# Performance work log

Hardware: AMD Instinct MI355X
Metric: run time of the kernel (lower is better)

## Reference

```python
import jax, jax.numpy as jnp
import numpy as np

N = 320   # batch of events
D = 64    # features per event
P = 1000  # permutation_count (hard-coded in module)


def setup_inputs() -> dict:
    key = jax.random.key(0)
    k1, k2, k3 = jax.random.split(key, 3)
    data = jax.random.normal(k1, (N, D), dtype=jnp.float32)
    particle_types = jax.random.randint(k2, (N,), 0, 2, dtype=jnp.int32)
    # quantum permutations: 1000 independent random permutations of [0, N)
    perms = jax.vmap(lambda k: jax.random.permutation(k, N))(jax.random.split(k3, P)).astype(jnp.int32)
    return {
        "data": data,
        "fermion_antisymmetry": jnp.float32(-1.0),
        "boson_symmetry": jnp.float32(1.0),
        "particle_types": particle_types,
        "perms": perms,
    }


def reference(data, fermion_antisymmetry, boson_symmetry, particle_types, perms):
    n = data.shape[0]
    tf = particle_types  # [n]
    # statistics factor matrix F[i,j]: fermion-fermion -> -1 param, boson-boson -> +1 param, mixed -> 1.0
    ff = (tf[:, None] == 0) & (tf[None, :] == 0)
    bb = (tf[:, None] == 1) & (tf[None, :] == 1)
    F = jnp.where(ff, fermion_antisymmetry, jnp.where(bb, boson_symmetry, jnp.float32(1.0)))  # [n,n]

    ar = jnp.arange(n)
    gathered = data[perms]                      # [P,n,d] = data[perm[i]]
    fac = F[ar[None, :], perms]                 # [P,n]   = F[i, perm[i]]
    same = perms == ar[None, :]                 # i == perm[i]: keep original row unscaled
    perm_data = jnp.where(same[..., None], gathered, fac[..., None] * gathered)  # [P,n,d]

    all_data = jnp.concatenate([data[None], perm_data], axis=0)  # [P+1,n,d]; row 0 = original

    # pairwise Euclidean norms via Gram trick (avoids [P+1,n,n,d] diff tensor)
    sn = jnp.sum(all_data * all_data, axis=-1)                   # [P+1,n]
    gram = jnp.einsum('pnd,pmd->pnm', all_data, all_data)        # [P+1,n,n]
    sq = jnp.maximum(sn[:, :, None] + sn[:, None, :] - 2.0 * gram, 0.0)

    iu, ju = jnp.triu_indices(n, k=1)
    vals = F[iu, ju][None, :] * jnp.sqrt(sq[:, iu, ju])          # [P+1, n*(n-1)/2]
    # torch.var default is unbiased (ddof=1)
    stats = jnp.var(vals, axis=1, ddof=1)                        # [P+1]
    return stats  # stats[0] = original test statistic, stats[1:] = permutation null distribution
```

## Files before the change

### kernel.cpp

```cpp
#include <hip/hip_runtime.h>
#include <math.h>

#define NN 320
#define DD 64
#define NPAIRF ((double)(NN * (NN - 1) / 2))

__global__ __launch_bounds__(NN) void gram_kernel(const float* __restrict__ data,
                                                  float* __restrict__ G) {
    __shared__ float rowa[DD];
    const int a = blockIdx.x;
    const int t = threadIdx.x;
    if (t < DD) rowa[t] = data[a * DD + t];
    __syncthreads();
    const float* rb = data + t * DD;
    float s = 0.f;
#pragma unroll
    for (int k = 0; k < DD; k += 4) {
        float4 x = *(const float4*)(rb + k);
        s = fmaf(rowa[k + 0], x.x, s);
        s = fmaf(rowa[k + 1], x.y, s);
        s = fmaf(rowa[k + 2], x.z, s);
        s = fmaf(rowa[k + 3], x.w, s);
    }
    G[a * NN + t] = s;
}

__global__ __launch_bounds__(512, 8) void perm_kernel(const float* __restrict__ G,
                                                      const int* __restrict__ types,
                                                      const int* __restrict__ perms,
                                                      const float* __restrict__ fermp,
                                                      const float* __restrict__ bosp,
                                                      float* __restrict__ out) {
    __shared__ __align__(16) float apk[NN * 4];
    __shared__ __align__(16) float colu[NN];
    __shared__ __align__(16) float colusn[NN];
    __shared__ __align__(16) float colvF[NN];
    __shared__ __align__(16) float colvB[NN];
    __shared__ double rsv[8], rsv2[8];

    const int p = blockIdx.x;
    const int t = threadIdx.x;
    const float Fv = *fermp;
    const float Bv = *bosp;
    const int* prow = (p == 0) ? (const int*)nullptr : perms + (size_t)(p - 1) * NN;

    for (int i = t; i < NN; i += 512) {
        const int a  = prow ? prow[i] : i;
        const int ti = types[i];
        const int ta = types[a];
        float uv = 1.0f;
        if (a != i) uv = (ti == 0 && ta == 0) ? Fv : ((ti == 1 && ta == 1) ? Bv : 1.0f);
        colu[a]  = uv;
        colvF[a] = (ti == 0) ? Fv : 1.0f;
        colvB[a] = (ti == 1) ? Bv : 1.0f;
        apk[4 * a + 0] = uv;
        apk[4 * a + 2] = -2.0f * uv;
        apk[4 * a + 3] = (float)ti;
    }
    __syncthreads();
    for (int a = t; a < NN; a += 512) {
        const float uv  = colu[a];
        const float usn = uv * uv * G[a * NN + a];
        colusn[a] = usn;
        apk[4 * a + 1] = usn;
    }
    __syncthreads();

    float accv = 0.0f, acc2 = 0.0f;

    const int strip  = t % 40;
    const int rowoff = t / 40;

    if (rowoff < 12) {
        const int col0 = strip * 8;
        const float4 ub0   = *(const float4*)(colu   + col0);
        const float4 ub1   = *(const float4*)(colu   + col0 + 4);
        const float4 usnb0 = *(const float4*)(colusn + col0);
        const float4 usnb1 = *(const float4*)(colusn + col0 + 4);
        const float4 vFb0  = *(const float4*)(colvF  + col0);
        const float4 vFb1  = *(const float4*)(colvF  + col0 + 4);
        const float4 vBb0  = *(const float4*)(colvB  + col0);
        const float4 vBb1  = *(const float4*)(colvB  + col0 + 4);

        const float* gp  = G + rowoff * NN + col0;
        const float* app = apk + 4 * rowoff;

#define PAIR_BODY(GC, UBC, USNBC, VFC, VBC)                      \
        {                                                        \
            const float tt  = (UBC) * (GC);                      \
            const float sab = ap.y + (USNBC);                    \
            const float d2  = fmaf(ap.z, tt, sab);               \
            const float dd  = __builtin_amdgcn_sqrtf(fabsf(d2)); \
            const float vsl = wa1 ? (VBC) : (VFC);               \
            accv = fmaf(vsl, dd, accv);                          \
            acc2 += fabsf(d2);                                   \
        }

#define ROW_BODY()                                               \
        {                                                        \
            const float4 ap = *(const float4*)app;               \
            const bool wa1 = (ap.w != 0.0f);                     \
            const float4 g0 = *(const float4*)gp;                \
            const float4 g1 = *(const float4*)(gp + 4);          \
            PAIR_BODY(g0.x, ub0.x, usnb0.x, vFb0.x, vBb0.x)      \
            PAIR_BODY(g0.y, ub0.y, usnb0.y, vFb0.y, vBb0.y)      \
            PAIR_BODY(g0.z, ub0.z, usnb0.z, vFb0.z, vBb0.z)      \
            PAIR_BODY(g0.w, ub0.w, usnb0.w, vFb0.w, vBb0.w)      \
            PAIR_BODY(g1.x, ub1.x, usnb1.x, vFb1.x, vBb1.x)      \
            PAIR_BODY(g1.y, ub1.y, usnb1.y, vFb1.y, vBb1.y)      \
            PAIR_BODY(g1.z, ub1.z, usnb1.z, vFb1.z, vBb1.z)      \
            PAIR_BODY(g1.w, ub1.w, usnb1.w, vFb1.w, vBb1.w)      \
        }

#pragma unroll 2
        for (int it = 0; it < 26; ++it) {
            ROW_BODY();
            gp  += 12 * NN;
            app += 48;
        }
        if (rowoff < 8) {
            ROW_BODY();
        }
#undef ROW_BODY
#undef PAIR_BODY
    }

    double sv = (double)accv, sv2 = (double)acc2;
    for (int off = 32; off; off >>= 1) {
        sv  += __shfl_down(sv, off, 64);
        sv2 += __shfl_down(sv2, off, 64);
    }
    const int wid = t >> 6, lane = t & 63;
    if (lane == 0) { rsv[wid] = sv; rsv2[wid] = sv2; }
    __syncthreads();
    if (t == 0) {
        double SV = 0.0, SV2 = 0.0;
#pragma unroll
        for (int i = 0; i < 8; ++i) { SV += rsv[i]; SV2 += rsv2[i]; }
        SV  *= 0.5;
        SV2 *= 0.5;
        const double var = (SV2 - SV * SV / NPAIRF) / (NPAIRF - 1.0);
        out[p] = (float)var;
    }
}

extern "C" void kernel_launch(void* const* d_in, const int* in_sizes, int n_in,
                              void* d_out, int out_size, void* d_ws, size_t ws_size,
                              hipStream_t stream) {
    const float* data  = (const float*)d_in[0];
    const float* fermp = (const float*)d_in[1];
    const float* bosp  = (const float*)d_in[2];
    const int*   types = (const int*)d_in[3];
    const int*   perms = (const int*)d_in[4];
    float* out = (float*)d_out;
    float* G   = (float*)d_ws;

    gram_kernel<<<NN, NN, 0, stream>>>(data, G);
    perm_kernel<<<1000 + 1, 512, 0, stream>>>(G, types, perms, fermp, bosp, out);
}
```

Measured before the change: 95.76 us.

## Process two permutations per block to reuse Gram loads and prefetch rows

Each block now evaluates two permutation configurations, so every Gram-matrix tile it loads serves both, which halves global G traffic per permutation and halves the block count. The row loop also prefetches the next G row into registers before computing the current one. In exchange, register use per thread roughly doubles (launch bounds relaxed to 4 blocks per SM) and the grid shrinks to 501 blocks, which lowers occupancy and parallelism.

```diff
diff --git a/kernel.cpp b/kernel.cpp
--- a/kernel.cpp
+++ b/kernel.cpp
@@ -25,122 +25,176 @@
     G[a * NN + t] = s;
 }
 
-__global__ __launch_bounds__(512, 8) void perm_kernel(const float* __restrict__ G,
+__global__ __launch_bounds__(512, 4) void perm_kernel(const float* __restrict__ G,
                                                       const int* __restrict__ types,
                                                       const int* __restrict__ perms,
                                                       const float* __restrict__ fermp,
                                                       const float* __restrict__ bosp,
                                                       float* __restrict__ out) {
-    __shared__ __align__(16) float apk[NN * 4];
-    __shared__ __align__(16) float colu[NN];
-    __shared__ __align__(16) float colusn[NN];
-    __shared__ __align__(16) float colvF[NN];
-    __shared__ __align__(16) float colvB[NN];
-    __shared__ double rsv[8], rsv2[8];
-
-    const int p = blockIdx.x;
-    const int t = threadIdx.x;
+    __shared__ __align__(16) float apkA[NN * 4];
+    __shared__ __align__(16) float apkB[NN * 4];
+    __shared__ __align__(16) float colu[2][NN];
+    __shared__ __align__(16) float colusn[2][NN];
+    __shared__ __align__(16) float colvF[2][NN];
+    __shared__ __align__(16) float colvB[2][NN];
+    __shared__ double rsv[2][8], rsv2[2][8];
+
+    const int blk = blockIdx.x;
+    const int t   = threadIdx.x;
     const float Fv = *fermp;
     const float Bv = *bosp;
-    const int* prow = (p == 0) ? (const int*)nullptr : perms + (size_t)(p - 1) * NN;
+
+    const int cfgA = 2 * blk;
+    const int cfgB = (2 * blk + 1 <= 1000) ? 2 * blk + 1 : 2 * blk;
+    const int* prowA = (cfgA == 0) ? (const int*)nullptr : perms + (size_t)(cfgA - 1) * NN;
+    const int* prowB = (cfgB == 0) ? (const int*)nullptr : perms + (size_t)(cfgB - 1) * NN;
 
     for (int i = t; i < NN; i += 512) {
-        const int a  = prow ? prow[i] : i;
         const int ti = types[i];
-        const int ta = types[a];
-        float uv = 1.0f;
-        if (a != i) uv = (ti == 0 && ta == 0) ? Fv : ((ti == 1 && ta == 1) ? Bv : 1.0f);
-        colu[a]  = uv;
-        colvF[a] = (ti == 0) ? Fv : 1.0f;
-        colvB[a] = (ti == 1) ? Bv : 1.0f;
-        apk[4 * a + 0] = uv;
-        apk[4 * a + 2] = -2.0f * uv;
-        apk[4 * a + 3] = (float)ti;
+        const float vF = (ti == 0) ? Fv : 1.0f;
+        const float vB = (ti == 1) ? Bv : 1.0f;
+        {
+            const int a = prowA ? prowA[i] : i;
+            float uv = 1.0f;
+            if (a != i) {
+                const int ta = types[a];
+                uv = (ti == 0 && ta == 0) ? Fv : ((ti == 1 && ta == 1) ? Bv : 1.0f);
+            }
+            colu[0][a] = uv; colvF[0][a] = vF; colvB[0][a] = vB;
+            apkA[4 * a + 0] = uv;
+            apkA[4 * a + 2] = -2.0f * uv;
+            apkA[4 * a + 3] = (float)ti;
+        }
+        {
+            const int a = prowB ? prowB[i] : i;
+            float uv = 1.0f;
+            if (a != i) {
+                const int ta = types[a];
+                uv = (ti == 0 && ta == 0) ? Fv : ((ti == 1 && ta == 1) ? Bv : 1.0f);
+            }
+            colu[1][a] = uv; colvF[1][a] = vF; colvB[1][a] = vB;
+            apkB[4 * a + 0] = uv;
+            apkB[4 * a + 2] = -2.0f * uv;
+            apkB[4 * a + 3] = (float)ti;
+        }
     }
     __syncthreads();
     for (int a = t; a < NN; a += 512) {
-        const float uv  = colu[a];
-        const float usn = uv * uv * G[a * NN + a];
-        colusn[a] = usn;
-        apk[4 * a + 1] = usn;
-    }
-    __syncthreads();
-
-    float accv = 0.0f, acc2 = 0.0f;
+        const float g = G[a * NN + a];
+        const float uA = colu[0][a], uB = colu[1][a];
+        const float usnA = uA * uA * g, usnB = uB * uB * g;
+        colusn[0][a] = usnA; apkA[4 * a + 1] = usnA;
+        colusn[1][a] = usnB; apkB[4 * a + 1] = usnB;
+    }
+    __syncthreads();
+
+    float accvA = 0.0f, acc2A = 0.0f, accvB = 0.0f, acc2B = 0.0f;
 
     const int strip  = t % 40;
     const int rowoff = t / 40;
 
     if (rowoff < 12) {
         const int col0 = strip * 8;
-        const float4 ub0   = *(const float4*)(colu   + col0);
-        const float4 ub1   = *(const float4*)(colu   + col0 + 4);
-        const float4 usnb0 = *(const float4*)(colusn + col0);
-        const float4 usnb1 = *(const float4*)(colusn + col0 + 4);
-        const float4 vFb0  = *(const float4*)(colvF  + col0);
-        const float4 vFb1  = *(const float4*)(colvF  + col0 + 4);
-        const float4 vBb0  = *(const float4*)(colvB  + col0);
-        const float4 vBb1  = *(const float4*)(colvB  + col0 + 4);
-
-        const float* gp  = G + rowoff * NN + col0;
-        const float* app = apk + 4 * rowoff;
-
-#define PAIR_BODY(GC, UBC, USNBC, VFC, VBC)                      \
+        const float4 uA0   = *(const float4*)(&colu[0][col0]);
+        const float4 uA1   = *(const float4*)(&colu[0][col0 + 4]);
+        const float4 snA0  = *(const float4*)(&colusn[0][col0]);
+        const float4 snA1  = *(const float4*)(&colusn[0][col0 + 4]);
+        const float4 vFA0  = *(const float4*)(&colvF[0][col0]);
+        const float4 vFA1  = *(const float4*)(&colvF[0][col0 + 4]);
+        const float4 vBA0  = *(const float4*)(&colvB[0][col0]);
+        const float4 vBA1  = *(const float4*)(&colvB[0][col0 + 4]);
+        const float4 uB0   = *(const float4*)(&colu[1][col0]);
+        const float4 uB1   = *(const float4*)(&colu[1][col0 + 4]);
+        const float4 snB0  = *(const float4*)(&colusn[1][col0]);
+        const float4 snB1  = *(const float4*)(&colusn[1][col0 + 4]);
+        const float4 vFB0  = *(const float4*)(&colvF[1][col0]);
+        const float4 vFB1  = *(const float4*)(&colvF[1][col0 + 4]);
+        const float4 vBB0  = *(const float4*)(&colvB[1][col0]);
+        const float4 vBB1  = *(const float4*)(&colvB[1][col0 + 4]);
+
+        const float* gp   = G + rowoff * NN + col0;
+        const float* appA = apkA + 4 * rowoff;
+        const float* appB = apkB + 4 * rowoff;
+
+        float4 g0 = *(const float4*)gp;
+        float4 g1 = *(const float4*)(gp + 4);
+
+#define PAIR(ACCV, ACC2, AP, WA, GC, UBC, SNBC, VFC, VBC)        \
         {                                                        \
             const float tt  = (UBC) * (GC);                      \
-            const float sab = ap.y + (USNBC);                    \
-            const float d2  = fmaf(ap.z, tt, sab);               \
+            const float sab = (AP).y + (SNBC);                   \
+            const float d2  = fmaf((AP).z, tt, sab);             \
             const float dd  = __builtin_amdgcn_sqrtf(fabsf(d2)); \
-            const float vsl = wa1 ? (VBC) : (VFC);               \
-            accv = fmaf(vsl, dd, accv);                          \
-            acc2 += fabsf(d2);                                   \
-        }
-
-#define ROW_BODY()                                               \
-        {                                                        \
-            const float4 ap = *(const float4*)app;               \
-            const bool wa1 = (ap.w != 0.0f);                     \
-            const float4 g0 = *(const float4*)gp;                \
-            const float4 g1 = *(const float4*)(gp + 4);          \
-            PAIR_BODY(g0.x, ub0.x, usnb0.x, vFb0.x, vBb0.x)      \
-            PAIR_BODY(g0.y, ub0.y, usnb0.y, vFb0.y, vBb0.y)      \
-            PAIR_BODY(g0.z, ub0.z, usnb0.z, vFb0.z, vBb0.z)      \
-            PAIR_BODY(g0.w, ub0.w, usnb0.w, vFb0.w, vBb0.w)      \
-            PAIR_BODY(g1.x, ub1.x, usnb1.x, vFb1.x, vBb1.x)      \
-            PAIR_BODY(g1.y, ub1.y, usnb1.y, vFb1.y, vBb1.y)      \
-            PAIR_BODY(g1.z, ub1.z, usnb1.z, vFb1.z, vBb1.z)      \
-            PAIR_BODY(g1.w, ub1.w, usnb1.w, vFb1.w, vBb1.w)      \
-        }
-
-#pragma unroll 2
+            const float vsl = (WA) ? (VBC) : (VFC);              \
+            ACCV = fmaf(vsl, dd, ACCV);                          \
+            ACC2 += fabsf(d2);                                   \
+        }
+
+#define ROW2()                                                           \
+        {                                                                \
+            const float4 apA = *(const float4*)appA;                     \
+            const float4 apB = *(const float4*)appB;                     \
+            const bool wA = (apA.w != 0.0f);                             \
+            const bool wB = (apB.w != 0.0f);                             \
+            PAIR(accvA, acc2A, apA, wA, g0.x, uA0.x, snA0.x, vFA0.x, vBA0.x) \
+            PAIR(accvA, acc2A, apA, wA, g0.y, uA0.y, snA0.y, vFA0.y, vBA0.y) \
+            PAIR(accvA, acc2A, apA, wA, g0.z, uA0.z, snA0.z, vFA0.z, vBA0.z) \
+            PAIR(accvA, acc2A, apA, wA, g0.w, uA0.w, snA0.w, vFA0.w, vBA0.w) \
+            PAIR(accvA, acc2A, apA, wA, g1.x, uA1.x, snA1.x, vFA1.x, vBA1.x) \
+            PAIR(accvA, acc2A, apA, wA, g1.y, uA1.y, snA1.y, vFA1.y, vBA1.y) \
+            PAIR(accvA, acc2A, apA, wA, g1.z, uA1.z, snA1.z, vFA1.z, vBA1.z) \
+            PAIR(accvA, acc2A, apA, wA, g1.w, uA1.w, snA1.w, vFA1.w, vBA1.w) \
+            PAIR(accvB, acc2B, apB, wB, g0.x, uB0.x, snB0.x, vFB0.x, vBB0.x) \
+            PAIR(accvB, acc2B, apB, wB, g0.y, uB0.y, snB0.y, vFB0.y, vBB0.y) \
+            PAIR(accvB, acc2B, apB, wB, g0.z, uB0.z, snB0.z, vFB0.z, vBB0.z) \
+            PAIR(accvB, acc2B, apB, wB, g0.w, uB0.w, snB0.w, vFB0.w, vBB0.w) \
+            PAIR(accvB, acc2B, apB, wB, g1.x, uB1.x, snB1.x, vFB1.x, vBB1.x) \
+            PAIR(accvB, acc2B, apB, wB, g1.y, uB1.y, snB1.y, vFB1.y, vBB1.y) \
+            PAIR(accvB, acc2B, apB, wB, g1.z, uB1.z, snB1.z, vFB1.z, vBB1.z) \
+            PAIR(accvB, acc2B, apB, wB, g1.w, uB1.w, snB1.w, vFB1.w, vBB1.w) \
+        }
+
         for (int it = 0; it < 26; ++it) {
-            ROW_BODY();
-            gp  += 12 * NN;
-            app += 48;
+            gp += 12 * NN;
+            const float4 n0 = *(const float4*)gp;
+            const float4 n1 = *(const float4*)(gp + 4);
+            ROW2();
+            appA += 48; appB += 48;
+            g0 = n0; g1 = n1;
         }
         if (rowoff < 8) {
-            ROW_BODY();
-        }
-#undef ROW_BODY
-#undef PAIR_BODY
-    }
-
-    double sv = (double)accv, sv2 = (double)acc2;
+            ROW2();
+        }
+#undef ROW2
+#undef PAIR
+    }
+
+    double svA = (double)accvA, sv2A = (double)acc2A;
+    double svB = (double)accvB, sv2B = (double)acc2B;
     for (int off = 32; off; off >>= 1) {
-        sv  += __shfl_down(sv, off, 64);
-        sv2 += __shfl_down(sv2, off, 64);
+        svA  += __shfl_down(svA,  off, 64);
+        sv2A += __shfl_down(sv2A, off, 64);
+        svB  += __shfl_down(svB,  off, 64);
+        sv2B += __shfl_down(sv2B, off, 64);
     }
     const int wid = t >> 6, lane = t & 63;
-    if (lane == 0) { rsv[wid] = sv; rsv2[wid] = sv2; }
+    if (lane == 0) {
+        rsv[0][wid] = svA; rsv2[0][wid] = sv2A;
+        rsv[1][wid] = svB; rsv2[1][wid] = sv2B;
+    }
     __syncthreads();
     if (t == 0) {
-        double SV = 0.0, SV2 = 0.0;
+        double SA = 0.0, S2A = 0.0, SB = 0.0, S2B = 0.0;
 #pragma unroll
-        for (int i = 0; i < 8; ++i) { SV += rsv[i]; SV2 += rsv2[i]; }
-        SV  *= 0.5;
-        SV2 *= 0.5;
-        const double var = (SV2 - SV * SV / NPAIRF) / (NPAIRF - 1.0);
-        out[p] = (float)var;
+        for (int i = 0; i < 8; ++i) {
+            SA += rsv[0][i]; S2A += rsv2[0][i];
+            SB += rsv[1][i]; S2B += rsv2[1][i];
+        }
+        SA *= 0.5; S2A *= 0.5;
+        SB *= 0.5; S2B *= 0.5;
+        out[cfgA] = (float)((S2A - SA * SA / NPAIRF) / (NPAIRF - 1.0));
+        if (2 * blk + 1 <= 1000)
+            out[cfgB] = (float)((S2B - SB * SB / NPAIRF) / (NPAIRF - 1.0));
     }
 }
 
@@ -156,5 +210,5 @@
     float* G   = (float*)d_ws;
 
     gram_kernel<<<NN, NN, 0, stream>>>(data, G);
-    perm_kernel<<<1000 + 1, 512, 0, stream>>>(G, types, perms, fermp, bosp, out);
+    perm_kernel<<<501, 512, 0, stream>>>(G, types, perms, fermp, bosp, out);
 }
```

Result: no change. 97.48 us (+1.8%).
